# Performance work log

Hardware: AMD Instinct MI355X
Metric: run time of the kernel (lower is better)

Reference implementation:

```python
import jax, jax.numpy as jnp
import numpy as np

H, W = 85, 85
N_HEAD = 8

def layernorm(x, g, b, eps=1e-5):
    m = x.mean(-1, keepdims=True)
    v = ((x - m) ** 2).mean(-1, keepdims=True)
    return (x - m) * jax.lax.rsqrt(v + eps) * g + b


def setup_inputs() -> dict:
    key = jax.random.key(0)
    ks = jax.random.split(key, 12)
    B, C = 8, 256
    N = H * W
    hd = C // N_HEAD
    Ch = C * 4  # mlp_ratio = 4
    init = lambda k, fan_in, sh: (jax.random.normal(k, sh, jnp.float32) / np.float32(np.sqrt(fan_in)))
    d = {}
    d['fx'] = jax.random.normal(ks[0], (B, N, C), jnp.float32)
    # ln_1
    d['ln1_g'] = jnp.ones((C,), jnp.float32); d['ln1_b'] = jnp.zeros((C,), jnp.float32)
    # Galerkin linear attention projections (per-head split of C)
    d['Wq'] = init(ks[1], C, (C, C)); d['bq'] = jnp.zeros((C,), jnp.float32)
    d['Wk'] = init(ks[2], C, (C, C)); d['bk'] = jnp.zeros((C,), jnp.float32)
    d['Wv'] = init(ks[3], C, (C, C)); d['bv'] = jnp.zeros((C,), jnp.float32)
    d['Wo'] = init(ks[4], C, (C, C)); d['bo'] = jnp.zeros((C,), jnp.float32)
    # per-head LayerNorms on K and V (Galerkin normalization replacing softmax)
    d['kln_g'] = jnp.ones((N_HEAD, hd), jnp.float32); d['kln_b'] = jnp.zeros((N_HEAD, hd), jnp.float32)
    d['vln_g'] = jnp.ones((N_HEAD, hd), jnp.float32); d['vln_b'] = jnp.zeros((N_HEAD, hd), jnp.float32)
    # ln_2
    d['ln2_g'] = jnp.ones((C,), jnp.float32); d['ln2_b'] = jnp.zeros((C,), jnp.float32)
    # MLP (n_layers=0, res=False): pre linear + gelu, post linear
    d['W1'] = init(ks[5], C, (C, Ch)); d['b1'] = jnp.zeros((Ch,), jnp.float32)
    d['W2'] = init(ks[6], Ch, (Ch, C)); d['b2'] = jnp.zeros((C,), jnp.float32)
    return d


def reference(fx, ln1_g, ln1_b, Wq, bq, Wk, bk, Wv, bv, Wo, bo,
              kln_g, kln_b, vln_g, vln_b, ln2_g, ln2_b, W1, b1, W2, b2):
    B, N, C = fx.shape
    hd = C // N_HEAD
    x = layernorm(fx, ln1_g, ln1_b)  # [B,N,C]
    # (permute/reshape to image grid and back is a no-op for per-token attention math)
    split = lambda t: t.reshape(B, N, N_HEAD, hd).transpose(0, 2, 1, 3)  # [B,h,N,d]
    q = split(x @ Wq + bq)
    k = split(x @ Wk + bk)
    v = split(x @ Wv + bv)
    # Galerkin: LayerNorm on K and V over head dim, no softmax
    k = layernorm(k, kln_g[None, :, None, :], kln_b[None, :, None, :])
    v = layernorm(v, vln_g[None, :, None, :], vln_b[None, :, None, :])
    kv = jnp.einsum('bhnd,bhne->bhde', k, v) / N  # [B,h,d,d]
    attn = jnp.einsum('bhnd,bhde->bhne', q, kv)   # [B,h,N,d]
    attn = attn.transpose(0, 2, 1, 3).reshape(B, N, C)
    attn = attn @ Wo + bo
    fx = fx + attn  # residual 1
    x2 = layernorm(fx, ln2_g, ln2_b)
    x2 = jax.nn.gelu(x2 @ W1 + b1) @ W2 + b2
    return fx + x2  # residual 2
```

## Files before the change

kernel.cpp:

```cpp
#include <hip/hip_runtime.h>
#include <hip/hip_bf16.h>
#include <stdint.h>

#define B_ 8
#define NTOK 7225
#define MTOT (B_*NTOK)
#define MROWS 58368
#define MT_FULL 226
#define MT_BATCH 29

typedef unsigned short u16;
typedef u16 u16x8 __attribute__((ext_vector_type(8)));
typedef u16 u16x4 __attribute__((ext_vector_type(4)));
typedef __bf16 bf16x8 __attribute__((ext_vector_type(8)));
typedef float f32x4 __attribute__((ext_vector_type(4)));

__device__ inline float bf2f(u16 u){ union{float f;uint32_t i;}c; c.i=((uint32_t)u)<<16; return c.f; }
__device__ inline u16 f2bf(float f){ union{float f;uint32_t i;}c; c.f=f; uint32_t x=c.i;
                                     return (u16)((x + 0x7fffu + ((x>>16)&1u))>>16); }
__device__ inline uint32_t cvt_pk_bf16(float a, float b){
  uint32_t r; asm("v_cvt_pk_bf16_f32 %0, %1, %2" : "=v"(r) : "v"(a), "v"(b)); return r;
}
__device__ inline float gelu_f(float x){
  float t = 0.7978845608028654f * x * (1.0f + 0.044715f*x*x);
  float e = __expf(2.0f*t);
  return x * (1.0f - __builtin_amdgcn_rcpf(e + 1.0f));
}

__device__ inline void gload_lds16(const u16* g, u16* l) {
  __builtin_amdgcn_global_load_lds(
      (__attribute__((address_space(1))) void*)(const_cast<u16*>(g)),
      (__attribute__((address_space(3))) void*)(l), 16, 0, 0);
}

template<int EPI>
__global__ __launch_bounds__(512, 2)
void gemm256(const u16* __restrict__ A, int lda,
             const u16* __restrict__ Bm, int ldb, long bStride,
             const float* __restrict__ bias, int biasStride,
             const float* __restrict__ res,
             void* __restrict__ outp, int ldo,
             int K, int rowsValid, int batchRowStride,
             const float* __restrict__ g2, const float* __restrict__ b2,
             u16* __restrict__ x2out)
{
  __shared__ alignas(16) u16 As[2][2][256][32];
  __shared__ alignas(16) u16 Bs[2][2][256][32];
  const int tid = threadIdx.x;
  const int wid = tid >> 6, lane = tid & 63;
  const int wm = wid >> 2, wn = wid & 3;

  const int gx = gridDim.x, gy = gridDim.y;
  const int n = gx * gy;
  const int flat = blockIdx.y * gx + blockIdx.x;
  const int qq = n >> 3, rr = n & 7;
  const int xcd = flat & 7, pos = flat >> 3;
  const int swz = (xcd < rr ? xcd*(qq+1) : rr*(qq+1) + (xcd-rr)*qq) + pos;
  const int bx = swz / gy, by = swz % gy;
  const int bz = blockIdx.z;

  const long rowBase = (long)bz * batchRowStride + (long)bx * 256;
  const int colBase = by * 256;
  const u16* Bp = Bm + (long)bz * bStride;
  const float* biasP = bias + bz * biasStride;

  const int srow = lane >> 2;
  const int scol = ((lane & 3) ^ ((lane >> 3) & 3)) * 8;
  const int NT = K >> 6;

  auto stageHalf = [&](int bf, int kt, int sel) {
    const int sub = sel >> 1;
    const int k0 = (kt << 6) + sub*32 + scol;
#pragma unroll
    for (int i = 0; i < 2; ++i) {
      const int r0 = (wid*2 + i)*16;
      if ((sel & 1) == 0)
        gload_lds16(A + (rowBase + r0 + srow)*(long)lda + k0, &As[bf][sub][r0][0]);
      else
        gload_lds16(Bp + (long)(colBase + r0 + srow)*ldb + k0, &Bs[bf][sub][r0][0]);
    }
  };

  f32x4 acc[8][4] = {};
  bf16x8 afr[4], bfr[4];
  const int lr = lane & 15;
  const int sl = lane >> 4;
  const int sp = (sl ^ ((lr >> 1) & 3)) * 8;

  stageHalf(0, 0, 0); stageHalf(0, 0, 1); stageHalf(0, 0, 2); stageHalf(0, 0, 3);
  asm volatile("s_waitcnt vmcnt(4)" ::: "memory");
  __builtin_amdgcn_s_barrier();

  for (int kt = 0; kt < NT; ++kt) {
    const int bf = kt & 1;
    const bool st = (kt + 1 < NT);
#pragma unroll
    for (int ph = 0; ph < 4; ++ph) {
      const int sub = ph >> 1, mh = ph & 1;
      if (mh == 0) {
#pragma unroll
        for (int ni = 0; ni < 4; ++ni)
          bfr[ni] = *reinterpret_cast<const bf16x8*>(&Bs[bf][sub][wn*64 + ni*16 + lr][sp]);
      }
#pragma unroll
      for (int i = 0; i < 4; ++i)
        afr[i] = *reinterpret_cast<const bf16x8*>(&As[bf][sub][wm*128 + (mh*4 + i)*16 + lr][sp]);
      if (st) stageHalf(bf ^ 1, kt + 1, ph);
      if (ph == 1) {
        if (st) asm volatile("s_waitcnt vmcnt(4)" ::: "memory");
        else    asm volatile("s_waitcnt vmcnt(0)" ::: "memory");
      } else if (ph == 3) {
        if (st) asm volatile("s_waitcnt vmcnt(4)" ::: "memory");
      }
      __builtin_amdgcn_sched_barrier(0);
      __builtin_amdgcn_s_barrier();
      asm volatile("s_waitcnt lgkmcnt(0)" ::: "memory");
      __builtin_amdgcn_sched_barrier(0);
      __builtin_amdgcn_s_setprio(1);
#pragma unroll
      for (int i = 0; i < 4; ++i)
#pragma unroll
        for (int ni = 0; ni < 4; ++ni)
          acc[mh*4 + i][ni] =
              __builtin_amdgcn_mfma_f32_16x16x32_bf16(bfr[ni], afr[i], acc[mh*4 + i][ni], 0, 0, 0);
      __builtin_amdgcn_s_setprio(0);
      __builtin_amdgcn_s_barrier();
    }
  }

  const int cq = sl * 4;
  if (EPI != 3) {
#pragma unroll
    for (int mi = 0; mi < 8; ++mi) {
      const int r = wm*128 + mi*16 + lr;
      if (bx*256 + r < rowsValid) {
        const long grow = rowBase + r;
#pragma unroll
        for (int ni = 0; ni < 4; ++ni) {
          const int c0 = colBase + wn*64 + ni*16 + cq;
          const long oidx = grow*(long)ldo + c0;
          f32x4 v = acc[mi][ni] + *reinterpret_cast<const f32x4*>(&biasP[c0]);
          if (EPI == 0) {
            uint2 pk; pk.x = cvt_pk_bf16(v[0], v[1]); pk.y = cvt_pk_bf16(v[2], v[3]);
            *reinterpret_cast<uint2*>((u16*)outp + oidx) = pk;
          } else if (EPI == 1) {
            uint2 pk; pk.x = cvt_pk_bf16(gelu_f(v[0]), gelu_f(v[1]));
            pk.y = cvt_pk_bf16(gelu_f(v[2]), gelu_f(v[3]));
            *reinterpret_cast<uint2*>((u16*)outp + oidx) = pk;
          } else {
            f32x4 rv = *reinterpret_cast<const f32x4*>((const float*)res + oidx);
            *reinterpret_cast<f32x4*>((float*)outp + oidx) = v + rv;
          }
        }
      }
    }
  } else {
    float* red = reinterpret_cast<float*>(&As[0][0][0][0]);
#pragma unroll
    for (int mi = 0; mi < 8; ++mi) {
      const int r = wm*128 + mi*16 + lr;
      const bool valid = (bx*256 + r < rowsValid);
      const long grow = rowBase + r;
      float s_r = 0.f, q_r = 0.f;
#pragma unroll
      for (int ni = 0; ni < 4; ++ni) {
        const int c0 = wn*64 + ni*16 + cq;
        f32x4 rv = valid ? *reinterpret_cast<const f32x4*>((const float*)res + grow*256 + c0)
                         : f32x4{0.f,0.f,0.f,0.f};
        f32x4 v = acc[mi][ni] + *reinterpret_cast<const f32x4*>(&biasP[c0]) + rv;
        acc[mi][ni] = v;
        s_r += v[0]+v[1]+v[2]+v[3];
        q_r += v[0]*v[0]+v[1]*v[1]+v[2]*v[2]+v[3]*v[3];
      }
      s_r += __shfl_xor(s_r, 16); s_r += __shfl_xor(s_r, 32);
      q_r += __shfl_xor(q_r, 16); q_r += __shfl_xor(q_r, 32);
      if (sl == 0) {
        red[       (wm*4 + wn)*128 + mi*16 + lr] = s_r;
        red[1024 + (wm*4 + wn)*128 + mi*16 + lr] = q_r;
      }
    }
    __syncthreads();
#pragma unroll
    for (int mi = 0; mi < 8; ++mi) {
      const int r = wm*128 + mi*16 + lr;
      if (bx*256 + r >= rowsValid) continue;
      const long grow = rowBase + r;
      const int rb = wm*4*128 + mi*16 + lr;
      float s_t = red[rb] + red[rb+128] + red[rb+256] + red[rb+384];
      float q_t = red[1024+rb] + red[1024+rb+128] + red[1024+rb+256] + red[1024+rb+384];
      const float m = s_t * (1.0f/256.0f);
      const float var = q_t * (1.0f/256.0f) - m*m;
      const float rs = rsqrtf(var + 1e-5f);
#pragma unroll
      for (int ni = 0; ni < 4; ++ni) {
        const int c0 = wn*64 + ni*16 + cq;
        const long oidx = grow*256 + c0;
        f32x4 v = acc[mi][ni];
        *reinterpret_cast<f32x4*>((float*)outp + oidx) = v;
        f32x4 gv = *reinterpret_cast<const f32x4*>(&g2[c0]);
        f32x4 bv = *reinterpret_cast<const f32x4*>(&b2[c0]);
        f32x4 xn = (v - m) * rs * gv + bv;
        uint2 pk; pk.x = cvt_pk_bf16(xn[0], xn[1]); pk.y = cvt_pk_bf16(xn[2], xn[3]);
        *reinterpret_cast<uint2*>(x2out + oidx) = pk;
      }
    }
  }
}

__global__ __launch_bounds__(256)
void ln_kernel(const float* __restrict__ in, const float* __restrict__ g,
               const float* __restrict__ bt, u16* __restrict__ out, int M)
{
  const int wv = threadIdx.x >> 6, lane = threadIdx.x & 63;
  const int t = blockIdx.x * 4 + wv;
  if (t >= M) return;
  const float4 x = reinterpret_cast<const float4*>(in + (long)t*256)[lane];
  float s = x.x + x.y + x.z + x.w;
  float q = x.x*x.x + x.y*x.y + x.z*x.z + x.w*x.w;
#pragma unroll
  for (int o = 32; o > 0; o >>= 1) { s += __shfl_xor(s, o); q += __shfl_xor(q, o); }
  const float m  = s * (1.0f/256.0f);
  const float var = q * (1.0f/256.0f) - m*m;
  const float rs = rsqrtf(var + 1e-5f);
  const float4 gv = reinterpret_cast<const float4*>(g)[lane];
  const float4 bv = reinterpret_cast<const float4*>(bt)[lane];
  uint2 o4;
  o4.x = cvt_pk_bf16((x.x - m)*rs*gv.x + bv.x, (x.y - m)*rs*gv.y + bv.y);
  o4.y = cvt_pk_bf16((x.z - m)*rs*gv.z + bv.z, (x.w - m)*rs*gv.w + bv.w);
  *reinterpret_cast<uint2*>(out + (long)t*256 + lane*4) = o4;
}

__global__ __launch_bounds__(256)
void kv_kernel(const u16* __restrict__ KV,
               const float* __restrict__ kg, const float* __restrict__ kb,
               const float* __restrict__ vg, const float* __restrict__ vb,
               float* __restrict__ kvout)
{
  const int bh = blockIdx.x, b = bh >> 3, h = bh & 7;
  const int tid = threadIdx.x;
  __shared__ u16 kls[256][32];
  __shared__ u16 vls[256][32];
  __shared__ float sg[4][32];
  if (tid < 32) {
    sg[0][tid] = kg[h*32 + tid];
    sg[1][tid] = kb[h*32 + tid];
    sg[2][tid] = vg[h*32 + tid];
    sg[3][tid] = vb[h*32 + tid];
  }
  const int d = tid >> 3, e0 = (tid & 7) * 4;
  float a0=0, a1=0, a2=0, a3=0;

  for (int sub = 0; sub < 2; ++sub) {
    const int r = blockIdx.y * 512 + sub * 256 + tid;
    __syncthreads();
    if (r < NTOK) {
      const u16* rowp = KV + (long)(b*NTOK + r)*512;
#pragma unroll
      for (int kv2 = 0; kv2 < 2; ++kv2) {
        const u16* p = rowp + (kv2 ? 256 : 0) + h*32;
        float xv[32]; float s = 0.f;
#pragma unroll
        for (int q4 = 0; q4 < 4; ++q4) {
          u16x8 u = *reinterpret_cast<const u16x8*>(p + q4*8);
#pragma unroll
          for (int j = 0; j < 8; ++j) { float f = bf2f(u[j]); xv[q4*8+j] = f; s += f; }
        }
        const float m = s * (1.0f/32.0f);
        float vv = 0.f;
#pragma unroll
        for (int j = 0; j < 32; ++j) { float d2 = xv[j]-m; vv += d2*d2; }
        const float rs = rsqrtf(vv*(1.0f/32.0f) + 1e-5f);
        const float* gg = sg[kv2 ? 2 : 0];
        const float* bb = sg[kv2 ? 3 : 1];
        u16 (*dst)[32] = kv2 ? vls : kls;
#pragma unroll
        for (int j = 0; j < 32; ++j) dst[tid][j] = f2bf((xv[j]-m)*rs*gg[j] + bb[j]);
      }
    } else {
#pragma unroll
      for (int j = 0; j < 32; ++j) { kls[tid][j] = 0; vls[tid][j] = 0; }
    }
    __syncthreads();
#pragma unroll 4
    for (int rr = 0; rr < 256; ++rr) {
      const float kd = bf2f(kls[rr][d]);
      u16x4 v4 = *reinterpret_cast<const u16x4*>(&vls[rr][e0]);
      a0 += kd * bf2f(v4[0]); a1 += kd * bf2f(v4[1]);
      a2 += kd * bf2f(v4[2]); a3 += kd * bf2f(v4[3]);
    }
  }
  const float sc = 1.0f / (float)NTOK;
  float* o = kvout + (long)bh*1024 + d*32 + e0;
  atomicAdd(o+0, a0*sc); atomicAdd(o+1, a1*sc);
  atomicAdd(o+2, a2*sc); atomicAdd(o+3, a3*sc);
}

__global__ __launch_bounds__(256)
void woeff_kernel(const float* __restrict__ kv, const float* __restrict__ Wo,
                  u16* __restrict__ Woet)
{
  const int b = blockIdx.x >> 8, c = blockIdx.x & 255;
  const int rtid = threadIdx.x;
  const int h = rtid >> 5, dd = rtid & 31;
  const float* kvp = kv + ((long)(b*8 + h)*32 + dd)*32;
  float s = 0.f;
#pragma unroll 8
  for (int e = 0; e < 32; ++e) s += kvp[e] * Wo[(h*32 + e)*256 + c];
  Woet[(long)(b*256 + c)*256 + rtid] = f2bf(s);
}

__global__ __launch_bounds__(256)
void watt_kernel(const u16* __restrict__ wq_bf, const u16* __restrict__ Woet,
                 u16* __restrict__ Watt)
{
  const int b = blockIdx.x >> 8, c = blockIdx.x & 255;
  const int k = threadIdx.x;
  const u16* wr = wq_bf + (long)k*256;
  const u16* er = Woet + ((long)(b*256 + c))*256;
  float s = 0.f;
#pragma unroll 4
  for (int j0 = 0; j0 < 256; j0 += 8) {
    u16x8 wv = *reinterpret_cast<const u16x8*>(wr + j0);
    u16x8 ev = *reinterpret_cast<const u16x8*>(er + j0);
#pragma unroll
    for (int j = 0; j < 8; ++j) s += bf2f(wv[j]) * bf2f(ev[j]);
  }
  Watt[((long)(b*256 + c))*256 + k] = f2bf(s);
}

__global__ __launch_bounds__(256)
void be_kernel(const float* __restrict__ bq, const float* __restrict__ bo,
               const u16* __restrict__ Woet, float* __restrict__ be)
{
  const int b = blockIdx.x, c = threadIdx.x;
  const u16* er = Woet + ((long)(b*256 + c))*256;
  float s = bo[c];
#pragma unroll 4
  for (int j0 = 0; j0 < 256; j0 += 8) {
    u16x8 ev = *reinterpret_cast<const u16x8*>(er + j0);
#pragma unroll
    for (int j = 0; j < 8; ++j) s += bq[j0+j] * bf2f(ev[j]);
  }
  be[b*256 + c] = s;
}

__device__ void transpose_tile(const float* __restrict__ src, u16* __restrict__ dst,
                               int R, int C, int tcx, int trY)
{
  __shared__ float t[32][33];
  const int tc = tcx * 32, tr = trY * 32;
  const int lx = threadIdx.x & 31, ly = threadIdx.x >> 5;
#pragma unroll
  for (int i = 0; i < 32; i += 8)
    t[ly + i][lx] = src[(long)(tr + ly + i)*C + tc + lx];
  __syncthreads();
#pragma unroll
  for (int i = 0; i < 32; i += 8)
    dst[(long)(tc + ly + i)*R + tr + lx] = f2bf(t[lx][ly + i]);
}

__global__ __launch_bounds__(256)
void prep_kernel(const float* __restrict__ Wk, const float* __restrict__ Wv,
                 const float* __restrict__ W1, const float* __restrict__ W2,
                 const float* __restrict__ Wq,
                 const float* __restrict__ bk, const float* __restrict__ bv,
                 u16* __restrict__ Wkv_t, u16* __restrict__ W1_t, u16* __restrict__ W2_t,
                 u16* __restrict__ wq_bf, float* __restrict__ kvb, float* __restrict__ bkv)
{
  int b = blockIdx.x;
  if (b < 256)      { transpose_tile(W1, W1_t, 256, 1024, b & 31, b >> 5); }
  else if (b < 512) { b -= 256; transpose_tile(W2, W2_t, 1024, 256, b & 7, b >> 3); }
  else if (b < 576) { b -= 512; transpose_tile(Wk, Wkv_t,         256, 256, b & 7, b >> 3); }
  else if (b < 640) { b -= 576; transpose_tile(Wv, Wkv_t + 65536, 256, 256, b & 7, b >> 3); }
  else if (b < 648) {
    const int base = (b - 640) * 8192 + threadIdx.x;
#pragma unroll
    for (int i = 0; i < 32; ++i) wq_bf[base + i*256] = f2bf(Wq[base + i*256]);
  } else if (b < 656) {
    const int base = (b - 648) * 8192 + threadIdx.x;
#pragma unroll
    for (int i = 0; i < 32; ++i) kvb[base + i*256] = 0.f;
  } else {
    const int i = threadIdx.x;
    bkv[i] = bk[i]; bkv[256 + i] = bv[i];
  }
}

extern "C" void kernel_launch(void* const* d_in, const int* in_sizes, int n_in,
                              void* d_out, int out_size, void* d_ws, size_t ws_size,
                              hipStream_t stream)
{
  const float* fx    = (const float*)d_in[0];
  const float* ln1_g = (const float*)d_in[1];
  const float* ln1_b = (const float*)d_in[2];
  const float* Wq = (const float*)d_in[3];
  const float* bq = (const float*)d_in[4];
  const float* Wk = (const float*)d_in[5];
  const float* bk = (const float*)d_in[6];
  const float* Wv = (const float*)d_in[7];
  const float* bv = (const float*)d_in[8];
  const float* Wo = (const float*)d_in[9];
  const float* bo = (const float*)d_in[10];
  const float* kg  = (const float*)d_in[11];
  const float* kbb = (const float*)d_in[12];
  const float* vg  = (const float*)d_in[13];
  const float* vbb = (const float*)d_in[14];
  const float* ln2_g = (const float*)d_in[15];
  const float* ln2_b = (const float*)d_in[16];
  const float* W1 = (const float*)d_in[17];
  const float* b1 = (const float*)d_in[18];
  const float* W2 = (const float*)d_in[19];
  const float* b2 = (const float*)d_in[20];
  float* outF = (float*)d_out;

  char* ws = (char*)d_ws;
  size_t off = 0;
  auto alloc = [&](size_t bytes) { char* p = ws + off; off += (bytes + 255) & ~(size_t)255; return p; };
  u16* bufX   = (u16*)alloc((size_t)MROWS*256*2);
  u16* bufKV  = (u16*)alloc((size_t)MROWS*512*2);
  u16* bufH   = (u16*)alloc((size_t)MROWS*1024*2);
  u16* Wkv_t  = (u16*)alloc(512*256*2);
  u16* W1_t   = (u16*)alloc(1024*256*2);
  u16* W2_t   = (u16*)alloc(256*1024*2);
  u16* Woe_t  = (u16*)alloc((size_t)8*256*256*2);
  u16* Watt   = (u16*)alloc((size_t)8*256*256*2);
  u16* wq_bf  = (u16*)alloc(256*256*2);
  float* kvb  = (float*)alloc((size_t)64*1024*4);
  float* bkv  = (float*)alloc(512*4);
  float* be   = (float*)alloc(8*256*4);
  (void)ws_size; (void)out_size; (void)n_in; (void)in_sizes;

  prep_kernel<<<657, 256, 0, stream>>>(Wk, Wv, W1, W2, Wq, bk, bv,
                                       Wkv_t, W1_t, W2_t, wq_bf, kvb, bkv);

  ln_kernel<<<MTOT/4, 256, 0, stream>>>(fx, ln1_g, ln1_b, bufX, MTOT);

  gemm256<0><<<dim3(MT_FULL, 2, 1), 512, 0, stream>>>(
      bufX, 256, Wkv_t, 256, 0, bkv, 0, nullptr, bufKV, 512, 256, MTOT, 0,
      nullptr, nullptr, nullptr);

  kv_kernel<<<dim3(64, 15), 256, 0, stream>>>(bufKV, kg, kbb, vg, vbb, kvb);

  woeff_kernel<<<2048, 256, 0, stream>>>(kvb, Wo, Woe_t);
  watt_kernel<<<2048, 256, 0, stream>>>(wq_bf, Woe_t, Watt);
  be_kernel<<<8, 256, 0, stream>>>(bq, bo, Woe_t, be);

  gemm256<3><<<dim3(MT_BATCH, 1, 8), 512, 0, stream>>>(
      bufX, 256, Watt, 256, 65536, be, 256, fx, outF, 256, 256, NTOK, NTOK,
      ln2_g, ln2_b, bufX);

  gemm256<1><<<dim3(MT_FULL, 4, 1), 512, 0, stream>>>(
      bufX, 256, W1_t, 256, 0, b1, 0, nullptr, bufH, 1024, 256, MTOT, 0,
      nullptr, nullptr, nullptr);

  gemm256<2><<<dim3(MT_FULL, 1, 1), 512, 0, stream>>>(
      bufH, 1024, W2_t, 1024, 0, b2, 0, outF, outF, 256, 1024, MTOT, 0,
      nullptr, nullptr, nullptr);
}
```

Baseline: 350.0 us.

## Fuse MLP up/down GEMMs into one kernel keeping hidden activations on chip

Replaces the two MLP GEMM launches with a single fused kernel. Each 64-row block computes the GELU hidden activations in 128-column chunks in LDS and accumulates the down projection directly, so the large bf16 hidden buffer is never written to or read from global memory. Weights are read straight from global or L2 without LDS staging, and the tiles are smaller, which may lower MFMA efficiency. Separately, the main GEMM pipeline moves its vmcnt waits and barrier to the start of each phase and drops the trailing barrier, which changes the load/compute overlap.

```diff
diff --git a/kernel.cpp b/kernel.cpp
--- a/kernel.cpp
+++ b/kernel.cpp
@@ -8,6 +8,7 @@
 #define MROWS 58368
 #define MT_FULL 226
 #define MT_BATCH 29
+#define MLP_TILES 904
 
 typedef unsigned short u16;
 typedef u16 u16x8 __attribute__((ext_vector_type(8)));
@@ -88,8 +89,6 @@
   const int sp = (sl ^ ((lr >> 1) & 3)) * 8;
 
   stageHalf(0, 0, 0); stageHalf(0, 0, 1); stageHalf(0, 0, 2); stageHalf(0, 0, 3);
-  asm volatile("s_waitcnt vmcnt(4)" ::: "memory");
-  __builtin_amdgcn_s_barrier();
 
   for (int kt = 0; kt < NT; ++kt) {
     const int bf = kt & 1;
@@ -97,6 +96,15 @@
 #pragma unroll
     for (int ph = 0; ph < 4; ++ph) {
       const int sub = ph >> 1, mh = ph & 1;
+      if (ph == 0) {
+        asm volatile("s_waitcnt vmcnt(4)" ::: "memory");
+      } else if (ph == 2) {
+        if (kt == NT - 1) asm volatile("s_waitcnt vmcnt(0)" ::: "memory");
+        else              asm volatile("s_waitcnt vmcnt(4)" ::: "memory");
+      } else {
+        asm volatile("s_waitcnt vmcnt(6)" ::: "memory");
+      }
+      __builtin_amdgcn_s_barrier();
       if (mh == 0) {
 #pragma unroll
         for (int ni = 0; ni < 4; ++ni)
@@ -106,14 +114,6 @@
       for (int i = 0; i < 4; ++i)
         afr[i] = *reinterpret_cast<const bf16x8*>(&As[bf][sub][wm*128 + (mh*4 + i)*16 + lr][sp]);
       if (st) stageHalf(bf ^ 1, kt + 1, ph);
-      if (ph == 1) {
-        if (st) asm volatile("s_waitcnt vmcnt(4)" ::: "memory");
-        else    asm volatile("s_waitcnt vmcnt(0)" ::: "memory");
-      } else if (ph == 3) {
-        if (st) asm volatile("s_waitcnt vmcnt(4)" ::: "memory");
-      }
-      __builtin_amdgcn_sched_barrier(0);
-      __builtin_amdgcn_s_barrier();
       asm volatile("s_waitcnt lgkmcnt(0)" ::: "memory");
       __builtin_amdgcn_sched_barrier(0);
       __builtin_amdgcn_s_setprio(1);
@@ -124,7 +124,6 @@
           acc[mh*4 + i][ni] =
               __builtin_amdgcn_mfma_f32_16x16x32_bf16(bfr[ni], afr[i], acc[mh*4 + i][ni], 0, 0, 0);
       __builtin_amdgcn_s_setprio(0);
-      __builtin_amdgcn_s_barrier();
     }
   }
 
@@ -142,10 +141,6 @@
           f32x4 v = acc[mi][ni] + *reinterpret_cast<const f32x4*>(&biasP[c0]);
           if (EPI == 0) {
             uint2 pk; pk.x = cvt_pk_bf16(v[0], v[1]); pk.y = cvt_pk_bf16(v[2], v[3]);
-            *reinterpret_cast<uint2*>((u16*)outp + oidx) = pk;
-          } else if (EPI == 1) {
-            uint2 pk; pk.x = cvt_pk_bf16(gelu_f(v[0]), gelu_f(v[1]));
-            pk.y = cvt_pk_bf16(gelu_f(v[2]), gelu_f(v[3]));
             *reinterpret_cast<uint2*>((u16*)outp + oidx) = pk;
           } else {
             f32x4 rv = *reinterpret_cast<const f32x4*>((const float*)res + oidx);
@@ -202,6 +197,112 @@
         f32x4 xn = (v - m) * rs * gv + bv;
         uint2 pk; pk.x = cvt_pk_bf16(xn[0], xn[1]); pk.y = cvt_pk_bf16(xn[2], xn[3]);
         *reinterpret_cast<uint2*>(x2out + oidx) = pk;
+      }
+    }
+  }
+}
+
+__global__ __launch_bounds__(256, 3)
+void mlp_fused(const u16* __restrict__ x2, const u16* __restrict__ W1t,
+               const u16* __restrict__ W2t, const float* __restrict__ b1,
+               const float* __restrict__ b2, float* __restrict__ outF,
+               int rowsValid)
+{
+  __shared__ alignas(16) u16 Xs[64][256];
+  __shared__ alignas(16) u16 Hs[64][128];
+  const int tid = threadIdx.x;
+  const int wid = tid >> 6, lane = tid & 63;
+  const int wm = wid >> 1, wn = wid & 1;
+  const int lr = lane & 15, sl = lane >> 4;
+  const long rowBase = (long)blockIdx.x * 64;
+
+#pragma unroll
+  for (int i = 0; i < 8; ++i) {
+    const int u = i*256 + tid;
+    const int r = u >> 5, slot = u & 31;
+    const int gc = ((slot ^ (r & 7)) << 3);
+    gload_lds16(x2 + (rowBase + r)*256 + gc, &Xs[r][slot*8]);
+  }
+  asm volatile("s_waitcnt vmcnt(0)" ::: "memory");
+  __builtin_amdgcn_s_barrier();
+
+  f32x4 acc2[2][8] = {};
+  for (int c = 0; c < 8; ++c) {
+    f32x4 acc1[2][4] = {};
+#pragma unroll 2
+    for (int kk = 0; kk < 8; ++kk) {
+      bf16x8 bfr[4], afr[2];
+#pragma unroll
+      for (int ni = 0; ni < 4; ++ni) {
+        const int hcol = c*128 + wn*64 + ni*16 + lr;
+        bfr[ni] = *reinterpret_cast<const bf16x8*>(&W1t[(long)hcol*256 + kk*32 + sl*8]);
+      }
+#pragma unroll
+      for (int mi = 0; mi < 2; ++mi) {
+        const int r = wm*32 + mi*16 + lr;
+        const int ps = ((kk*4 + sl) ^ (r & 7)) * 8;
+        afr[mi] = *reinterpret_cast<const bf16x8*>(&Xs[r][ps]);
+      }
+#pragma unroll
+      for (int mi = 0; mi < 2; ++mi)
+#pragma unroll
+        for (int ni = 0; ni < 4; ++ni)
+          acc1[mi][ni] = __builtin_amdgcn_mfma_f32_16x16x32_bf16(bfr[ni], afr[mi], acc1[mi][ni], 0, 0, 0);
+    }
+    if (c > 0) __builtin_amdgcn_s_barrier();
+    const float* b1c = b1 + c*128;
+#pragma unroll
+    for (int mi = 0; mi < 2; ++mi) {
+      const int r = wm*32 + mi*16 + lr;
+#pragma unroll
+      for (int ni = 0; ni < 4; ++ni) {
+        const int col = wn*64 + ni*16 + sl*4;
+        f32x4 v = acc1[mi][ni] + *reinterpret_cast<const f32x4*>(&b1c[col]);
+        uint2 pk; pk.x = cvt_pk_bf16(gelu_f(v[0]), gelu_f(v[1]));
+        pk.y = cvt_pk_bf16(gelu_f(v[2]), gelu_f(v[3]));
+        const int u8 = (col >> 2) ^ ((r & 7) << 1);
+        *reinterpret_cast<uint2*>(&Hs[r][u8*4]) = pk;
+      }
+    }
+    __builtin_amdgcn_s_barrier();
+#pragma unroll
+    for (int kk2 = 0; kk2 < 4; ++kk2) {
+      bf16x8 af2[2];
+#pragma unroll
+      for (int mi = 0; mi < 2; ++mi) {
+        const int r = wm*32 + mi*16 + lr;
+        const int u8 = (kk2*8 + sl*2) ^ ((r & 7) << 1);
+        af2[mi] = *reinterpret_cast<const bf16x8*>(&Hs[r][u8*4]);
+      }
+#pragma unroll
+      for (int ng = 0; ng < 2; ++ng) {
+        bf16x8 bf2[4];
+#pragma unroll
+        for (int nj = 0; nj < 4; ++nj) {
+          const int ocol = wn*128 + (ng*4 + nj)*16 + lr;
+          bf2[nj] = *reinterpret_cast<const bf16x8*>(&W2t[(long)ocol*1024 + c*128 + kk2*32 + sl*8]);
+        }
+#pragma unroll
+        for (int mi = 0; mi < 2; ++mi)
+#pragma unroll
+          for (int nj = 0; nj < 4; ++nj)
+            acc2[mi][ng*4 + nj] =
+                __builtin_amdgcn_mfma_f32_16x16x32_bf16(bf2[nj], af2[mi], acc2[mi][ng*4 + nj], 0, 0, 0);
+      }
+    }
+  }
+#pragma unroll
+  for (int mi = 0; mi < 2; ++mi) {
+    const int r = wm*32 + mi*16 + lr;
+    const long grow = rowBase + r;
+    if (grow < rowsValid) {
+#pragma unroll
+      for (int ni = 0; ni < 8; ++ni) {
+        const int col = wn*128 + ni*16 + sl*4;
+        const long oidx = grow*256 + col;
+        f32x4 v = acc2[mi][ni] + *reinterpret_cast<const f32x4*>(&b2[col])
+                + *reinterpret_cast<const f32x4*>(&outF[oidx]);
+        *reinterpret_cast<f32x4*>(&outF[oidx]) = v;
       }
     }
   }
@@ -418,7 +519,6 @@
   auto alloc = [&](size_t bytes) { char* p = ws + off; off += (bytes + 255) & ~(size_t)255; return p; };
   u16* bufX   = (u16*)alloc((size_t)MROWS*256*2);
   u16* bufKV  = (u16*)alloc((size_t)MROWS*512*2);
-  u16* bufH   = (u16*)alloc((size_t)MROWS*1024*2);
   u16* Wkv_t  = (u16*)alloc(512*256*2);
   u16* W1_t   = (u16*)alloc(1024*256*2);
   u16* W2_t   = (u16*)alloc(256*1024*2);
@@ -449,11 +549,5 @@
       bufX, 256, Watt, 256, 65536, be, 256, fx, outF, 256, 256, NTOK, NTOK,
       ln2_g, ln2_b, bufX);
 
-  gemm256<1><<<dim3(MT_FULL, 4, 1), 512, 0, stream>>>(
-      bufX, 256, W1_t, 256, 0, b1, 0, nullptr, bufH, 1024, 256, MTOT, 0,
-      nullptr, nullptr, nullptr);
-
-  gemm256<2><<<dim3(MT_FULL, 1, 1), 512, 0, stream>>>(
-      bufH, 1024, W2_t, 1024, 0, b2, 0, outF, outF, 256, 1024, MTOT, 0,
-      nullptr, nullptr, nullptr);
-}
+  mlp_fused<<<MLP_TILES, 256, 0, stream>>>(bufX, W1_t, W2_t, b1, b2, outF, MTOT);
+}
```

Result: slower. 473.1 us (+35.2%).

## Halve per-phase barriers in GEMM loop and coalesce bf16 epilogue via LDS

Applied to the files above, without the earlier changes.

Moves the vmcnt wait and barrier ahead of the LDS fragment reads and removes the trailing barrier after each MFMA phase, so each phase syncs only once. Replaces the separate A/B shared arrays with one flat LDS buffer. In the bf16 and gelu epilogues, the output tile is staged through swizzled LDS so each row is written as contiguous 16-byte stores. The restructured waits need correct vmcnt accounting to avoid races, and the coalesced store no longer checks rowsValid, so it relies on padded output rows.

```diff
diff --git a/kernel.cpp b/kernel.cpp
--- a/kernel.cpp
+++ b/kernel.cpp
@@ -44,8 +44,7 @@
              const float* __restrict__ g2, const float* __restrict__ b2,
              u16* __restrict__ x2out)
 {
-  __shared__ alignas(16) u16 As[2][2][256][32];
-  __shared__ alignas(16) u16 Bs[2][2][256][32];
+  __shared__ alignas(16) u16 lds[65536];
   const int tid = threadIdx.x;
   const int wid = tid >> 6, lane = tid & 63;
   const int wm = wid >> 2, wn = wid & 3;
@@ -71,13 +70,14 @@
   auto stageHalf = [&](int bf, int kt, int sel) {
     const int sub = sel >> 1;
     const int k0 = (kt << 6) + sub*32 + scol;
+    u16* base = lds + ((sel & 1) ? 32768 : 0) + (bf*2 + sub)*8192;
 #pragma unroll
     for (int i = 0; i < 2; ++i) {
       const int r0 = (wid*2 + i)*16;
       if ((sel & 1) == 0)
-        gload_lds16(A + (rowBase + r0 + srow)*(long)lda + k0, &As[bf][sub][r0][0]);
+        gload_lds16(A + (rowBase + r0 + srow)*(long)lda + k0, base + r0*32);
       else
-        gload_lds16(Bp + (long)(colBase + r0 + srow)*ldb + k0, &Bs[bf][sub][r0][0]);
+        gload_lds16(Bp + (long)(colBase + r0 + srow)*ldb + k0, base + r0*32);
     }
   };
 
@@ -88,8 +88,6 @@
   const int sp = (sl ^ ((lr >> 1) & 3)) * 8;
 
   stageHalf(0, 0, 0); stageHalf(0, 0, 1); stageHalf(0, 0, 2); stageHalf(0, 0, 3);
-  asm volatile("s_waitcnt vmcnt(4)" ::: "memory");
-  __builtin_amdgcn_s_barrier();
 
   for (int kt = 0; kt < NT; ++kt) {
     const int bf = kt & 1;
@@ -97,23 +95,26 @@
 #pragma unroll
     for (int ph = 0; ph < 4; ++ph) {
       const int sub = ph >> 1, mh = ph & 1;
+      if (ph == 0) {
+        asm volatile("s_waitcnt vmcnt(4)" ::: "memory");
+      } else if (ph == 2) {
+        if (kt == NT - 1) asm volatile("s_waitcnt vmcnt(0)" ::: "memory");
+        else              asm volatile("s_waitcnt vmcnt(4)" ::: "memory");
+      } else {
+        asm volatile("s_waitcnt vmcnt(6)" ::: "memory");
+      }
+      __builtin_amdgcn_s_barrier();
+      const u16* Ab = lds + (bf*2 + sub)*8192;
+      const u16* Bb = lds + 32768 + (bf*2 + sub)*8192;
       if (mh == 0) {
 #pragma unroll
         for (int ni = 0; ni < 4; ++ni)
-          bfr[ni] = *reinterpret_cast<const bf16x8*>(&Bs[bf][sub][wn*64 + ni*16 + lr][sp]);
+          bfr[ni] = *reinterpret_cast<const bf16x8*>(&Bb[(wn*64 + ni*16 + lr)*32 + sp]);
       }
 #pragma unroll
       for (int i = 0; i < 4; ++i)
-        afr[i] = *reinterpret_cast<const bf16x8*>(&As[bf][sub][wm*128 + (mh*4 + i)*16 + lr][sp]);
+        afr[i] = *reinterpret_cast<const bf16x8*>(&Ab[(wm*128 + (mh*4 + i)*16 + lr)*32 + sp]);
       if (st) stageHalf(bf ^ 1, kt + 1, ph);
-      if (ph == 1) {
-        if (st) asm volatile("s_waitcnt vmcnt(4)" ::: "memory");
-        else    asm volatile("s_waitcnt vmcnt(0)" ::: "memory");
-      } else if (ph == 3) {
-        if (st) asm volatile("s_waitcnt vmcnt(4)" ::: "memory");
-      }
-      __builtin_amdgcn_sched_barrier(0);
-      __builtin_amdgcn_s_barrier();
       asm volatile("s_waitcnt lgkmcnt(0)" ::: "memory");
       __builtin_amdgcn_sched_barrier(0);
       __builtin_amdgcn_s_setprio(1);
@@ -124,12 +125,37 @@
           acc[mh*4 + i][ni] =
               __builtin_amdgcn_mfma_f32_16x16x32_bf16(bfr[ni], afr[i], acc[mh*4 + i][ni], 0, 0, 0);
       __builtin_amdgcn_s_setprio(0);
-      __builtin_amdgcn_s_barrier();
     }
   }
 
   const int cq = sl * 4;
-  if (EPI != 3) {
+  if (EPI <= 1) {
+    __syncthreads();
+#pragma unroll
+    for (int mi = 0; mi < 8; ++mi) {
+      const int r = wm*128 + mi*16 + lr;
+#pragma unroll
+      for (int ni = 0; ni < 4; ++ni) {
+        const int c = wn*64 + ni*16 + cq;
+        f32x4 v = acc[mi][ni] + *reinterpret_cast<const f32x4*>(&biasP[colBase + c]);
+        uint2 pk;
+        if (EPI == 1) { pk.x = cvt_pk_bf16(gelu_f(v[0]), gelu_f(v[1]));
+                        pk.y = cvt_pk_bf16(gelu_f(v[2]), gelu_f(v[3])); }
+        else          { pk.x = cvt_pk_bf16(v[0], v[1]); pk.y = cvt_pk_bf16(v[2], v[3]); }
+        const int unit = ((c >> 3) ^ (r & 7));
+        *reinterpret_cast<uint2*>(lds + r*256 + unit*8 + (c & 7)) = pk;
+      }
+    }
+    __syncthreads();
+#pragma unroll
+    for (int p = 0; p < 16; ++p) {
+      const int idx = p*512 + tid;
+      const int r = idx >> 5, u = idx & 31;
+      const int phys = u ^ (r & 7);
+      u16x8 val = *reinterpret_cast<const u16x8*>(lds + r*256 + phys*8);
+      *reinterpret_cast<u16x8*>((u16*)outp + (rowBase + r)*(long)ldo + colBase + u*8) = val;
+    }
+  } else if (EPI == 2) {
 #pragma unroll
     for (int mi = 0; mi < 8; ++mi) {
       const int r = wm*128 + mi*16 + lr;
@@ -140,22 +166,14 @@
           const int c0 = colBase + wn*64 + ni*16 + cq;
           const long oidx = grow*(long)ldo + c0;
           f32x4 v = acc[mi][ni] + *reinterpret_cast<const f32x4*>(&biasP[c0]);
-          if (EPI == 0) {
-            uint2 pk; pk.x = cvt_pk_bf16(v[0], v[1]); pk.y = cvt_pk_bf16(v[2], v[3]);
-            *reinterpret_cast<uint2*>((u16*)outp + oidx) = pk;
-          } else if (EPI == 1) {
-            uint2 pk; pk.x = cvt_pk_bf16(gelu_f(v[0]), gelu_f(v[1]));
-            pk.y = cvt_pk_bf16(gelu_f(v[2]), gelu_f(v[3]));
-            *reinterpret_cast<uint2*>((u16*)outp + oidx) = pk;
-          } else {
-            f32x4 rv = *reinterpret_cast<const f32x4*>((const float*)res + oidx);
-            *reinterpret_cast<f32x4*>((float*)outp + oidx) = v + rv;
-          }
+          f32x4 rv = *reinterpret_cast<const f32x4*>((const float*)res + oidx);
+          *reinterpret_cast<f32x4*>((float*)outp + oidx) = v + rv;
         }
       }
     }
   } else {
-    float* red = reinterpret_cast<float*>(&As[0][0][0][0]);
+    float* red = reinterpret_cast<float*>(lds);
+    __syncthreads();
 #pragma unroll
     for (int mi = 0; mi < 8; ++mi) {
       const int r = wm*128 + mi*16 + lr;
```

After: 328.5 us. 1.07x faster.
